# Performance work log

Measured on AMD Instinct MI355X. Metric: run time of the kernel, lower is better.

## Reference

```python
import jax, jax.numpy as jnp
import numpy as np

B, S, K_IN = 8, 2048, 512
D_MODEL, N_INPUT, N_PROCESS = 1024, 4096, 2048
K = 256


def setup_inputs() -> dict:
    key = jax.random.key(0)
    k1, k2, k3, k4 = jax.random.split(key, 4)
    return {
        "selected_activations": jax.random.normal(k1, (B, S, K_IN), dtype=jnp.float32),
        "selected_indices": jax.random.randint(k2, (B, K_IN), 0, N_INPUT, dtype=jnp.int64),
        "k": K,
        "combination_weights": jax.random.normal(k3, (N_PROCESS, N_INPUT), dtype=jnp.float32),
        "output_projections": jax.random.normal(k4, (N_PROCESS, D_MODEL), dtype=jnp.float32),
    }


def reference(selected_activations, selected_indices, k, combination_weights, output_projections):
    # Gather per-batch combination weights: [n_process, B, k_in] -> [B, n_process, k_in]
    sel_w = jnp.take(combination_weights, selected_indices, axis=1)  # [P, B, k_in]
    sel_w = jnp.transpose(sel_w, (1, 0, 2))                          # [B, P, k_in]
    # Batched matmul + exact GELU (torch F.gelu default is erf-based)
    process_act = jax.nn.gelu(
        jnp.einsum("bsk,bpk->bsp", selected_activations, sel_w), approximate=False
    )  # [B, S, P]
    # Top-k gating over mean activation across sequence
    process_scores = process_act.mean(axis=1)                        # [B, P]
    _, proc_idx = jax.lax.top_k(process_scores, k)                   # [B, k]
    # Gather selected process activations along last dim
    sel_proc_act = jnp.take_along_axis(process_act, proc_idx[:, None, :], axis=2)  # [B, S, k]
    # Gather output projections per batch: [B, k, d_model]
    sel_proj = output_projections[proc_idx]                          # [B, k, D]
    return jnp.einsum("bsk,bkd->bsd", sel_proc_act, sel_proj)        # [B, S, D]
```

## Files before the change

kernel.cpp:

```cpp
#include <hip/hip_runtime.h>
#include <hip/hip_bf16.h>
#include <math.h>

#define B_    8
#define S_    2048
#define KIN_  512
#define NIN_  4096
#define P_    2048
#define D_    1024
#define KSEL_ 256

typedef __attribute__((ext_vector_type(8))) short short8;
typedef __attribute__((ext_vector_type(4))) float f32x4;

__device__ __forceinline__ unsigned short f2bf(float f) {
    unsigned u = __float_as_uint(f);
    unsigned r = (u + 0x7fffu + ((u >> 16) & 1u)) >> 16;
    return (unsigned short)r;
}
__device__ __forceinline__ float bf2f(unsigned short h) {
    return __uint_as_float(((unsigned)h) << 16);
}
__device__ __forceinline__ float gelu_exact(float x) {
    return 0.5f * x * (1.0f + erff(x * 0.70710678118654752f));
}
__device__ __forceinline__ void gl2lds16(const void* g, void* l) {
    __builtin_amdgcn_global_load_lds(
        (const __attribute__((address_space(1))) unsigned int*)g,
        (__attribute__((address_space(3))) unsigned int*)l, 16, 0, 0);
}

__global__ __launch_bounds__(256) void prep_kernel(
        const float* __restrict__ A, const float* __restrict__ W,
        const int* __restrict__ idx,
        unsigned short* __restrict__ Ahi, unsigned short* __restrict__ Alo,
        unsigned short* __restrict__ Ghi, unsigned short* __restrict__ Glo) {
    int id = blockIdx.x;
    int t  = threadIdx.x;
    if (id < 1024) {
        int b = id >> 7, rb = id & 127;
        int l = t & 63, wv = t >> 6;
        int lr = l & 15, quad = l >> 4;
        const float* src = A + ((size_t)(b * S_ + rb * 16 + lr)) * KIN_ + quad * 8;
        unsigned short* dh = Ahi + ((size_t)(b * S_ + rb * 16 + lr)) * KIN_ + quad * 8;
        unsigned short* dl = Alo + (size_t)(b * 16) * 65536 + (size_t)rb * 512 + (size_t)l * 8;
        for (int kb = wv; kb < 16; kb += 4) {
            float4 v0 = *(const float4*)(src + kb * 32);
            float4 v1 = *(const float4*)(src + kb * 32 + 4);
            float vv[8] = {v0.x, v0.y, v0.z, v0.w, v1.x, v1.y, v1.z, v1.w};
            short8 h8, l8;
#pragma unroll
            for (int jj = 0; jj < 8; jj++) {
                unsigned short h = f2bf(vv[jj]);
                h8[jj] = (short)h;
                l8[jj] = (short)f2bf(vv[jj] - bf2f(h));
            }
            *(short8*)(dh + kb * 32) = h8;
            *(short8*)(dl + (size_t)kb * 65536) = l8;
        }
    } else {
        int bp = id - 1024;
        int b  = bp >> 11;
        const int* ib = idx + (size_t)b * KIN_;
        const float* wrow = W + (size_t)(bp & 2047) * NIN_;
        size_t o = (size_t)bp * KIN_;
        for (int j = t; j < KIN_; j += 256) {
            float v = wrow[ib[j]];
            unsigned short h = f2bf(v);
            Ghi[o + j] = h;
            Glo[o + j] = f2bf(v - bf2f(h));
        }
    }
}

template <bool STORE_C>
__global__ __launch_bounds__(256, 3) void gemm1_score(
        const unsigned short* __restrict__ Ahi, const unsigned short* __restrict__ Alo,
        const unsigned short* __restrict__ Ghi, const unsigned short* __restrict__ Glo,
        float* __restrict__ scores, unsigned short* __restrict__ C) {
    __shared__ __align__(16) unsigned short lds[24576];

    int d    = blockIdx.x;
    int xcd  = d & 7;
    int slot = d >> 3;
    int c    = (slot >> 4) * 8 + xcd;
    int j    = slot & 15;
    int b    = c >> 4;
    int rc   = c & 15;
    int p0   = ((rc & 3) * 4 + (j & 3)) * 128;
    int s0   = ((rc >> 2) * 4 + (j >> 2)) * 128;

    const int t  = threadIdx.x;
    const int w = t >> 6, l = t & 63;
    const int wm = w & 1, wn = w >> 1;
    const int lr = l & 15, quad = l >> 4;

    const int srow = t >> 2;
    const int koff = ((t & 3) ^ ((t >> 3) & 3)) * 8;
    const size_t baseA = ((size_t)(b * S_ + s0)) * KIN_;
    const size_t baseG = ((size_t)(b * P_ + p0)) * KIN_;
    const unsigned short* pA0 = Ahi + baseA + (size_t)srow * KIN_ + koff;
    const unsigned short* pA1 = pA0 + (size_t)64 * KIN_;
    const unsigned short* pG0 = Ghi + baseG + (size_t)srow * KIN_ + koff;
    const unsigned short* pG1 = pG0 + (size_t)64 * KIN_;
    const unsigned short* pH0 = Glo + baseG + (size_t)srow * KIN_ + koff;
    const unsigned short* pH1 = pH0 + (size_t)64 * KIN_;
    const unsigned short* alB = Alo + (size_t)(b * 16) * 65536
                              + (size_t)((s0 >> 4) + wm * 4) * 512 + (size_t)l * 8;
    char* lb = (char*)lds + w * 1024;

    int ra[4], rg[4];
#pragma unroll
    for (int i = 0; i < 4; i++) {
        int rowa = wm * 64 + i * 16 + lr;
        int rowg = wn * 64 + i * 16 + lr;
        ra[i] = rowa * 32 + (quad ^ ((rowa >> 1) & 3)) * 8;
        rg[i] = rowg * 32 + (quad ^ ((rowg >> 1) & 3)) * 8;
    }

    f32x4 acc[4][4];
#pragma unroll
    for (int i = 0; i < 4; i++)
#pragma unroll
        for (int jj = 0; jj < 4; jj++) acc[i][jj] = (f32x4){0.f, 0.f, 0.f, 0.f};

    auto issue = [&](int k0, int buf) {
        char* dst = lb + buf * 24576;
        gl2lds16(pA0 + k0, dst + 0);
        gl2lds16(pA1 + k0, dst + 4096);
        gl2lds16(pG0 + k0, dst + 8192);
        gl2lds16(pG1 + k0, dst + 12288);
        gl2lds16(pH0 + k0, dst + 16384);
        gl2lds16(pH1 + k0, dst + 20480);
    };

    issue(0, 0);
    for (int it = 0; it < KIN_ / 32; ++it) {
        short8 alc[4];
#pragma unroll
        for (int mt = 0; mt < 4; mt++)
            alc[mt] = *(const short8*)(alB + (size_t)it * 65536 + mt * 512);
        if (it + 1 < KIN_ / 32) {
            issue((it + 1) * 32, (it + 1) & 1);
            asm volatile("s_waitcnt vmcnt(10)\n\ts_barrier" ::: "memory");
        } else {
            asm volatile("s_waitcnt vmcnt(0)\n\ts_barrier" ::: "memory");
        }
        const unsigned short* Lb = lds + (it & 1) * 12288;

        short8 gh[4], gl8[4];
#pragma unroll
        for (int i = 0; i < 4; i++) {
            gh[i]  = *(const short8*)(Lb + 4096 + rg[i]);
            gl8[i] = *(const short8*)(Lb + 8192 + rg[i]);
        }
#pragma unroll
        for (int mt = 0; mt < 4; mt++) {
            short8 ah = *(const short8*)(Lb + ra[mt]);
#pragma unroll
            for (int nt = 0; nt < 4; nt++) {
                acc[mt][nt] = __builtin_amdgcn_mfma_f32_16x16x32_bf16(ah,      gh[nt],  acc[mt][nt], 0, 0, 0);
                acc[mt][nt] = __builtin_amdgcn_mfma_f32_16x16x32_bf16(ah,      gl8[nt], acc[mt][nt], 0, 0, 0);
                acc[mt][nt] = __builtin_amdgcn_mfma_f32_16x16x32_bf16(alc[mt], gh[nt],  acc[mt][nt], 0, 0, 0);
            }
        }
        asm volatile("s_barrier" ::: "memory");
    }

    float colsum[4] = {0.f, 0.f, 0.f, 0.f};
#pragma unroll
    for (int mt = 0; mt < 4; mt++)
#pragma unroll
        for (int nt = 0; nt < 4; nt++)
#pragma unroll
            for (int r = 0; r < 4; r++) {
                float g = gelu_exact(acc[mt][nt][r]);
                colsum[nt] += g;
                acc[mt][nt][r] = g;
            }
#pragma unroll
    for (int nt = 0; nt < 4; nt++) {
        colsum[nt] += __shfl_xor(colsum[nt], 16);
        colsum[nt] += __shfl_xor(colsum[nt], 32);
    }
    if (quad == 0) {
#pragma unroll
        for (int nt = 0; nt < 4; nt++)
            atomicAdd(&scores[b * P_ + p0 + wn * 64 + nt * 16 + lr], colsum[nt]);
    }

    if (STORE_C) {
#pragma unroll
        for (int mt = 0; mt < 4; mt++)
#pragma unroll
            for (int nt = 0; nt < 4; nt++)
#pragma unroll
                for (int r = 0; r < 4; r++) {
                    int row = wm * 64 + mt * 16 + quad * 4 + r;
                    int col = wn * 64 + nt * 16 + lr;
                    lds[row * 128 + col] = f2bf(acc[mt][nt][r]);
                }
        __syncthreads();
        for (int i = t; i < 2048; i += 256) {
            int row = i >> 4, ch = i & 15;
            uint4 v = *(const uint4*)(lds + row * 128 + ch * 8);
            *(uint4*)(C + ((size_t)(b * S_ + s0 + row)) * P_ + p0 + ch * 8) = v;
        }
    }
}

__global__ __launch_bounds__(1024) void topk_kernel(const float* __restrict__ scores,
                                                    int* __restrict__ pidx) {
    __shared__ float v[2048];
    __shared__ int   ix[2048];
    int b = blockIdx.x;
    int t = threadIdx.x;
    for (int i = t; i < 2048; i += 1024) { v[i] = scores[b * 2048 + i]; ix[i] = i; }
    __syncthreads();
    for (int k = 2; k <= 2048; k <<= 1) {
        for (int j = k >> 1; j > 0; j >>= 1) {
            for (int i = t; i < 2048; i += 1024) {
                int o = i ^ j;
                if (o > i) {
                    bool desc = ((i & k) == 0);
                    float va = v[i], vb = v[o];
                    int ia = ix[i], ib = ix[o];
                    bool b_first = (vb > va) || (vb == va && ib < ia);
                    if (desc == b_first) { v[i] = vb; v[o] = va; ix[i] = ib; ix[o] = ia; }
                }
            }
            __syncthreads();
        }
    }
    if (t < KSEL_) pidx[b * KSEL_ + t] = ix[t];
}

__global__ __launch_bounds__(256) void gathers_kernel(
        const unsigned short* __restrict__ C, const float* __restrict__ proj,
        const int* __restrict__ pidx,
        unsigned short* __restrict__ selact, unsigned short* __restrict__ PselT,
        int base) {
    __shared__ int pj[256];
    __shared__ unsigned short tile[64][65];
    int id = blockIdx.x + base, t = threadIdx.x;
    if (id < 2048) {
        int b = id >> 8;
        pj[t] = pidx[b * KSEL_ + t];
        __syncthreads();
        size_t r0 = (size_t)b * S_ + (id & 255) * 8;
#pragma unroll
        for (int r = 0; r < 8; ++r) {
            size_t row = r0 + r;
            selact[row * KSEL_ + t] = C[row * P_ + pj[t]];
        }
    } else {
        int g = id - 2048;
        int d0 = (g & 15) * 64, k0 = ((g >> 4) & 3) * 64, b = g >> 6;
        int tr = t >> 6;
        int tc = t & 63;
#pragma unroll
        for (int r = 0; r < 16; r++) {
            int kk = r * 4 + tr;
            int prow = pidx[b * KSEL_ + k0 + kk];
            tile[kk][tc] = f2bf(proj[(size_t)prow * D_ + d0 + tc]);
        }
        __syncthreads();
#pragma unroll
        for (int r = 0; r < 16; r++) {
            int dd = r * 4 + tr;
            PselT[((size_t)(b * D_ + d0 + dd)) * KSEL_ + k0 + tc] = tile[tc][dd];
        }
    }
}

__global__ __launch_bounds__(256) void gemm1b_selact(
        const unsigned short* __restrict__ Ahi, const unsigned short* __restrict__ Alo,
        const unsigned short* __restrict__ Ghi, const unsigned short* __restrict__ Glo,
        const int* __restrict__ pidx, unsigned short* __restrict__ selact) {
    __shared__ __align__(16) unsigned short lds[16384];

    const int t  = threadIdx.x;
    const int b  = blockIdx.z;
    const int s0 = blockIdx.y * 128;
    const int n0 = blockIdx.x * 128;
    const int w = t >> 6, l = t & 63;
    const int wm = w & 1, wn = w >> 1;
    const int lr = l & 15, quad = l >> 4;

    const int srow = t >> 2;
    const int koff = ((t & 3) ^ ((t >> 3) & 3)) * 8;
    const size_t baseA = ((size_t)(b * S_ + s0)) * KIN_;
    const size_t offA0 = baseA + (size_t)srow * KIN_ + koff;
    const size_t offA1 = offA0 + (size_t)64 * KIN_;
    const int prow0 = pidx[b * KSEL_ + n0 + srow];
    const int prow1 = pidx[b * KSEL_ + n0 + 64 + srow];
    const size_t offG0 = ((size_t)(b * P_ + prow0)) * KIN_ + koff;
    const size_t offG1 = ((size_t)(b * P_ + prow1)) * KIN_ + koff;
    const unsigned short* alB = Alo + (size_t)(b * 16) * 65536
                              + (size_t)((s0 >> 4) + wm * 4) * 512 + (size_t)l * 8;
    char* lb = (char*)lds + w * 1024;

    int ra[4], rg[4];
#pragma unroll
    for (int i = 0; i < 4; i++) {
        int rowa = wm * 64 + i * 16 + lr;
        int rowg = wn * 64 + i * 16 + lr;
        ra[i] = rowa * 32 + (quad ^ ((rowa >> 1) & 3)) * 8;
        rg[i] = rowg * 32 + (quad ^ ((rowg >> 1) & 3)) * 8;
    }

    f32x4 acc[4][4];
#pragma unroll
    for (int i = 0; i < 4; i++)
#pragma unroll
        for (int jj = 0; jj < 4; jj++) acc[i][jj] = (f32x4){0.f, 0.f, 0.f, 0.f};

    for (int k0 = 0; k0 < KIN_; k0 += 32) {
        gl2lds16(Ahi + offA0 + k0, lb + 0);
        gl2lds16(Ahi + offA1 + k0, lb + 4096);
        gl2lds16(Ghi + offG0 + k0, lb + 8192);
        gl2lds16(Ghi + offG1 + k0, lb + 12288);
        gl2lds16(Glo + offG0 + k0, lb + 16384);
        gl2lds16(Glo + offG1 + k0, lb + 20480);
        short8 alc[4];
#pragma unroll
        for (int mt = 0; mt < 4; mt++)
            alc[mt] = *(const short8*)(alB + (size_t)(k0 >> 5) * 65536 + mt * 512);
        __syncthreads();

        short8 gh[4], gl8[4];
#pragma unroll
        for (int i = 0; i < 4; i++) {
            gh[i]  = *(const short8*)(lds + 4096 + rg[i]);
            gl8[i] = *(const short8*)(lds + 8192 + rg[i]);
        }
#pragma unroll
        for (int mt = 0; mt < 4; mt++) {
            short8 ah = *(const short8*)(lds + ra[mt]);
#pragma unroll
            for (int nt = 0; nt < 4; nt++) {
                acc[mt][nt] = __builtin_amdgcn_mfma_f32_16x16x32_bf16(ah,      gh[nt],  acc[mt][nt], 0, 0, 0);
                acc[mt][nt] = __builtin_amdgcn_mfma_f32_16x16x32_bf16(ah,      gl8[nt], acc[mt][nt], 0, 0, 0);
                acc[mt][nt] = __builtin_amdgcn_mfma_f32_16x16x32_bf16(alc[mt], gh[nt],  acc[mt][nt], 0, 0, 0);
            }
        }
        __syncthreads();
    }

#pragma unroll
    for (int mt = 0; mt < 4; mt++)
#pragma unroll
        for (int nt = 0; nt < 4; nt++)
#pragma unroll
            for (int r = 0; r < 4; r++) {
                int row = wm * 64 + mt * 16 + quad * 4 + r;
                int col = wn * 64 + nt * 16 + lr;
                lds[row * 128 + col] = f2bf(gelu_exact(acc[mt][nt][r]));
            }
    __syncthreads();
    for (int i = t; i < 2048; i += 256) {
        int row = i >> 4, ch = i & 15;
        uint4 v = *(const uint4*)(lds + row * 128 + ch * 8);
        *(uint4*)(selact + ((size_t)(b * S_ + s0 + row)) * KSEL_ + n0 + ch * 8) = v;
    }
}

__global__ __launch_bounds__(256) void gemm2_mfma(
        const unsigned short* __restrict__ selact,
        const unsigned short* __restrict__ PselT,
        float* __restrict__ out) {
    __shared__ __align__(16) unsigned short lds[16384];

    const int t  = threadIdx.x;
    const int b  = blockIdx.z;
    const int s0 = blockIdx.y * 128;
    const int d0 = blockIdx.x * 128;
    const int w = t >> 6, l = t & 63;
    const int wm = w & 1, wn = w >> 1;
    const int lr = l & 15, quad = l >> 4;

    const int srow = t >> 2;
    const int koff = ((t & 3) ^ ((t >> 3) & 3)) * 8;
    const unsigned short* pA0 = selact + ((size_t)(b * S_ + s0 + srow)) * KSEL_ + koff;
    const unsigned short* pA1 = pA0 + (size_t)64 * KSEL_;
    const unsigned short* pB0 = PselT + ((size_t)(b * D_ + d0 + srow)) * KSEL_ + koff;
    const unsigned short* pB1 = pB0 + (size_t)64 * KSEL_;
    char* lb = (char*)lds + w * 1024;

    int ra[4], rg[4];
#pragma unroll
    for (int i = 0; i < 4; i++) {
        int rowa = wm * 64 + i * 16 + lr;
        int rowg = wn * 64 + i * 16 + lr;
        ra[i] = rowa * 32 + (quad ^ ((rowa >> 1) & 3)) * 8;
        rg[i] = rowg * 32 + (quad ^ ((rowg >> 1) & 3)) * 8;
    }

    f32x4 acc[4][4];
#pragma unroll
    for (int i = 0; i < 4; i++)
#pragma unroll
        for (int jj = 0; jj < 4; jj++) acc[i][jj] = (f32x4){0.f, 0.f, 0.f, 0.f};

    auto issue = [&](int k0, int buf) {
        char* dst = lb + buf * 16384;
        gl2lds16(pA0 + k0, dst + 0);
        gl2lds16(pA1 + k0, dst + 4096);
        gl2lds16(pB0 + k0, dst + 8192);
        gl2lds16(pB1 + k0, dst + 12288);
    };

    issue(0, 0);
    for (int it = 0; it < KSEL_ / 32; ++it) {
        if (it + 1 < KSEL_ / 32) {
            issue((it + 1) * 32, (it + 1) & 1);
            asm volatile("s_waitcnt vmcnt(4)\n\ts_barrier" ::: "memory");
        } else {
            asm volatile("s_waitcnt vmcnt(0)\n\ts_barrier" ::: "memory");
        }
        const unsigned short* Lb = lds + (it & 1) * 8192;

        short8 af[4], bf[4];
#pragma unroll
        for (int i = 0; i < 4; i++) {
            af[i] = *(const short8*)(Lb + ra[i]);
            bf[i] = *(const short8*)(Lb + 4096 + rg[i]);
        }
#pragma unroll
        for (int mt = 0; mt < 4; mt++)
#pragma unroll
            for (int nt = 0; nt < 4; nt++)
                acc[mt][nt] = __builtin_amdgcn_mfma_f32_16x16x32_bf16(af[mt], bf[nt], acc[mt][nt], 0, 0, 0);
        asm volatile("s_barrier" ::: "memory");
    }

#pragma unroll
    for (int mt = 0; mt < 4; mt++)
#pragma unroll
        for (int nt = 0; nt < 4; nt++)
#pragma unroll
            for (int r = 0; r < 4; r++)
                out[((size_t)(b * S_ + s0 + wm * 64 + mt * 16 + quad * 4 + r)) * D_
                    + d0 + wn * 64 + nt * 16 + lr] = acc[mt][nt][r];
}

extern "C" void kernel_launch(void* const* d_in, const int* in_sizes, int n_in,
                              void* d_out, int out_size, void* d_ws, size_t ws_size,
                              hipStream_t stream) {
    (void)in_sizes; (void)n_in; (void)out_size;
    const float* act  = (const float*)d_in[0];
    const int*   idx  = (const int*)d_in[1];
    const float* W    = (const float*)d_in[3];
    const float* proj = (const float*)d_in[4];
    float*       out  = (float*)d_out;

    char* ws = (char*)d_ws;
    unsigned short* Ahi    = (unsigned short*)(ws + 0);
    unsigned short* Alo    = (unsigned short*)(ws + 16777216);
    unsigned short* Ghi    = (unsigned short*)(ws + 33554432);
    unsigned short* Glo    = (unsigned short*)(ws + 50331648);
    float*          scores = (float*)(ws + 67108864);
    int*            pidx   = (int*)(ws + 67174400);
    unsigned short* selact = (unsigned short*)(ws + 67182592);
    unsigned short* PselT  = (unsigned short*)(ws + 75571200);
    unsigned short* Cbf    = (unsigned short*)(ws + 79765504);
    const bool big = ws_size >= 146874368ull;

    hipMemsetAsync(scores, 0, B_ * P_ * sizeof(float), stream);

    prep_kernel<<<dim3(1024 + B_ * P_), 256, 0, stream>>>(act, W, idx, Ahi, Alo, Ghi, Glo);

    if (big) {
        gemm1_score<true><<<dim3(2048), 256, 0, stream>>>(Ahi, Alo, Ghi, Glo, scores, Cbf);
        topk_kernel<<<dim3(B_), 1024, 0, stream>>>(scores, pidx);
        gathers_kernel<<<dim3(2048 + 512), 256, 0, stream>>>(Cbf, proj, pidx, selact, PselT, 0);
    } else {
        gemm1_score<false><<<dim3(2048), 256, 0, stream>>>(Ahi, Alo, Ghi, Glo, scores, nullptr);
        topk_kernel<<<dim3(B_), 1024, 0, stream>>>(scores, pidx);
        gemm1b_selact<<<dim3(KSEL_ / 128, S_ / 128, B_), 256, 0, stream>>>(
            Ahi, Alo, Ghi, Glo, pidx, selact);
        gathers_kernel<<<dim3(512), 256, 0, stream>>>(Cbf, proj, pidx, selact, PselT, 2048);
    }
    gemm2_mfma<<<dim3(D_ / 128, S_ / 128, B_), 256, 0, stream>>>(selact, PselT, out);
}
```

Measured before the change: 364.0 us.

## Store G low-part in MFMA fragment layout and load it directly to registers

```diff
diff --git a/kernel.cpp b/kernel.cpp
--- a/kernel.cpp
+++ b/kernel.cpp
@@ -30,11 +30,13 @@
         (__attribute__((address_space(3))) unsigned int*)l, 16, 0, 0);
 }
 
+
 __global__ __launch_bounds__(256) void prep_kernel(
         const float* __restrict__ A, const float* __restrict__ W,
         const int* __restrict__ idx,
-        unsigned short* __restrict__ Ahi, unsigned short* __restrict__ Alo,
-        unsigned short* __restrict__ Ghi, unsigned short* __restrict__ Glo) {
+        unsigned short* __restrict__ Ahi, unsigned short* __restrict__ AloF,
+        unsigned short* __restrict__ Ghi, unsigned short* __restrict__ GloF) {
+    __shared__ int ibs[KIN_];
     int id = blockIdx.x;
     int t  = threadIdx.x;
     if (id < 1024) {
@@ -43,7 +45,7 @@
         int lr = l & 15, quad = l >> 4;
         const float* src = A + ((size_t)(b * S_ + rb * 16 + lr)) * KIN_ + quad * 8;
         unsigned short* dh = Ahi + ((size_t)(b * S_ + rb * 16 + lr)) * KIN_ + quad * 8;
-        unsigned short* dl = Alo + (size_t)(b * 16) * 65536 + (size_t)rb * 512 + (size_t)l * 8;
+        unsigned short* dl = AloF + (size_t)b * 1048576 + (size_t)rb * 512 + (size_t)l * 8;
         for (int kb = wv; kb < 16; kb += 4) {
             float4 v0 = *(const float4*)(src + kb * 32);
             float4 v1 = *(const float4*)(src + kb * 32 + 4);
@@ -59,26 +61,37 @@
             *(short8*)(dl + (size_t)kb * 65536) = l8;
         }
     } else {
-        int bp = id - 1024;
-        int b  = bp >> 11;
-        const int* ib = idx + (size_t)b * KIN_;
-        const float* wrow = W + (size_t)(bp & 2047) * NIN_;
-        size_t o = (size_t)bp * KIN_;
-        for (int j = t; j < KIN_; j += 256) {
-            float v = wrow[ib[j]];
+        int g = id - 1024;
+        int b = g >> 9;
+        ibs[t]       = idx[b * KIN_ + t];
+        ibs[t + 256] = idx[b * KIN_ + t + 256];
+        __syncthreads();
+        int wv = t >> 6, tt = t & 63;
+        int p  = (g * 4 + wv) & 2047;
+        const float* wrow = W + (size_t)p * NIN_;
+        size_t o = ((size_t)b * P_ + p) * KIN_;
+        unsigned short* gf = GloF + (size_t)b * 1048576 + (size_t)(tt >> 2) * 65536
+                           + (size_t)(p >> 4) * 512
+                           + (size_t)((tt & 3) * 16 + (p & 15)) * 8;
+        short8 h8, l8;
+#pragma unroll
+        for (int e = 0; e < 8; e++) {
+            float v = wrow[ibs[tt * 8 + e]];
             unsigned short h = f2bf(v);
-            Ghi[o + j] = h;
-            Glo[o + j] = f2bf(v - bf2f(h));
-        }
+            h8[e] = (short)h;
+            l8[e] = (short)f2bf(v - bf2f(h));
+        }
+        *(short8*)(Ghi + o + tt * 8) = h8;
+        *(short8*)gf = l8;
     }
 }
 
 template <bool STORE_C>
-__global__ __launch_bounds__(256, 3) void gemm1_score(
-        const unsigned short* __restrict__ Ahi, const unsigned short* __restrict__ Alo,
-        const unsigned short* __restrict__ Ghi, const unsigned short* __restrict__ Glo,
+__global__ __launch_bounds__(256, 4) void gemm1_score(
+        const unsigned short* __restrict__ Ahi, const unsigned short* __restrict__ AloF,
+        const unsigned short* __restrict__ Ghi, const unsigned short* __restrict__ GloF,
         float* __restrict__ scores, unsigned short* __restrict__ C) {
-    __shared__ __align__(16) unsigned short lds[24576];
+    __shared__ __align__(16) unsigned short lds[16384];
 
     int d    = blockIdx.x;
     int xcd  = d & 7;
@@ -103,10 +116,10 @@
     const unsigned short* pA1 = pA0 + (size_t)64 * KIN_;
     const unsigned short* pG0 = Ghi + baseG + (size_t)srow * KIN_ + koff;
     const unsigned short* pG1 = pG0 + (size_t)64 * KIN_;
-    const unsigned short* pH0 = Glo + baseG + (size_t)srow * KIN_ + koff;
-    const unsigned short* pH1 = pH0 + (size_t)64 * KIN_;
-    const unsigned short* alB = Alo + (size_t)(b * 16) * 65536
+    const unsigned short* alB = AloF + (size_t)b * 1048576
                               + (size_t)((s0 >> 4) + wm * 4) * 512 + (size_t)l * 8;
+    const unsigned short* glB = GloF + (size_t)b * 1048576
+                              + (size_t)((p0 >> 4) + wn * 4) * 512 + (size_t)l * 8;
     char* lb = (char*)lds + w * 1024;
 
     int ra[4], rg[4];
@@ -125,42 +138,39 @@
         for (int jj = 0; jj < 4; jj++) acc[i][jj] = (f32x4){0.f, 0.f, 0.f, 0.f};
 
     auto issue = [&](int k0, int buf) {
-        char* dst = lb + buf * 24576;
+        char* dst = lb + buf * 16384;
         gl2lds16(pA0 + k0, dst + 0);
         gl2lds16(pA1 + k0, dst + 4096);
         gl2lds16(pG0 + k0, dst + 8192);
         gl2lds16(pG1 + k0, dst + 12288);
-        gl2lds16(pH0 + k0, dst + 16384);
-        gl2lds16(pH1 + k0, dst + 20480);
     };
 
     issue(0, 0);
     for (int it = 0; it < KIN_ / 32; ++it) {
-        short8 alc[4];
-#pragma unroll
-        for (int mt = 0; mt < 4; mt++)
-            alc[mt] = *(const short8*)(alB + (size_t)it * 65536 + mt * 512);
+        short8 alc[4], glc[4];
+#pragma unroll
+        for (int i = 0; i < 4; i++) {
+            alc[i] = *(const short8*)(alB + (size_t)it * 65536 + i * 512);
+            glc[i] = *(const short8*)(glB + (size_t)it * 65536 + i * 512);
+        }
         if (it + 1 < KIN_ / 32) {
             issue((it + 1) * 32, (it + 1) & 1);
-            asm volatile("s_waitcnt vmcnt(10)\n\ts_barrier" ::: "memory");
+            asm volatile("s_waitcnt vmcnt(12)\n\ts_barrier" ::: "memory");
         } else {
-            asm volatile("s_waitcnt vmcnt(0)\n\ts_barrier" ::: "memory");
-        }
-        const unsigned short* Lb = lds + (it & 1) * 12288;
-
-        short8 gh[4], gl8[4];
-#pragma unroll
-        for (int i = 0; i < 4; i++) {
-            gh[i]  = *(const short8*)(Lb + 4096 + rg[i]);
-            gl8[i] = *(const short8*)(Lb + 8192 + rg[i]);
-        }
+            asm volatile("s_waitcnt vmcnt(8)\n\ts_barrier" ::: "memory");
+        }
+        const unsigned short* Lb = lds + (it & 1) * 8192;
+
+        short8 gh[4];
+#pragma unroll
+        for (int i = 0; i < 4; i++) gh[i] = *(const short8*)(Lb + 4096 + rg[i]);
 #pragma unroll
         for (int mt = 0; mt < 4; mt++) {
             short8 ah = *(const short8*)(Lb + ra[mt]);
 #pragma unroll
             for (int nt = 0; nt < 4; nt++) {
                 acc[mt][nt] = __builtin_amdgcn_mfma_f32_16x16x32_bf16(ah,      gh[nt],  acc[mt][nt], 0, 0, 0);
-                acc[mt][nt] = __builtin_amdgcn_mfma_f32_16x16x32_bf16(ah,      gl8[nt], acc[mt][nt], 0, 0, 0);
+                acc[mt][nt] = __builtin_amdgcn_mfma_f32_16x16x32_bf16(ah,      glc[nt], acc[mt][nt], 0, 0, 0);
                 acc[mt][nt] = __builtin_amdgcn_mfma_f32_16x16x32_bf16(alc[mt], gh[nt],  acc[mt][nt], 0, 0, 0);
             }
         }
@@ -274,8 +284,8 @@
 }
 
 __global__ __launch_bounds__(256) void gemm1b_selact(
-        const unsigned short* __restrict__ Ahi, const unsigned short* __restrict__ Alo,
-        const unsigned short* __restrict__ Ghi, const unsigned short* __restrict__ Glo,
+        const unsigned short* __restrict__ Ahi, const unsigned short* __restrict__ AloF,
+        const unsigned short* __restrict__ Ghi, const unsigned short* __restrict__ GloF,
         const int* __restrict__ pidx, unsigned short* __restrict__ selact) {
     __shared__ __align__(16) unsigned short lds[16384];
 
@@ -296,8 +306,15 @@
     const int prow1 = pidx[b * KSEL_ + n0 + 64 + srow];
     const size_t offG0 = ((size_t)(b * P_ + prow0)) * KIN_ + koff;
     const size_t offG1 = ((size_t)(b * P_ + prow1)) * KIN_ + koff;
-    const unsigned short* alB = Alo + (size_t)(b * 16) * 65536
+    const unsigned short* alB = AloF + (size_t)b * 1048576
                               + (size_t)((s0 >> 4) + wm * 4) * 512 + (size_t)l * 8;
+    const unsigned short* glb = GloF + (size_t)b * 1048576;
+    size_t gloff[4];
+#pragma unroll
+    for (int i = 0; i < 4; i++) {
+        int pp = pidx[b * KSEL_ + n0 + wn * 64 + i * 16 + lr];
+        gloff[i] = (size_t)(pp >> 4) * 512 + (size_t)(quad * 16 + (pp & 15)) * 8;
+    }
     char* lb = (char*)lds + w * 1024;
 
     int ra[4], rg[4];
@@ -316,31 +333,29 @@
         for (int jj = 0; jj < 4; jj++) acc[i][jj] = (f32x4){0.f, 0.f, 0.f, 0.f};
 
     for (int k0 = 0; k0 < KIN_; k0 += 32) {
+        int kb = k0 >> 5;
         gl2lds16(Ahi + offA0 + k0, lb + 0);
         gl2lds16(Ahi + offA1 + k0, lb + 4096);
         gl2lds16(Ghi + offG0 + k0, lb + 8192);
         gl2lds16(Ghi + offG1 + k0, lb + 12288);
-        gl2lds16(Glo + offG0 + k0, lb + 16384);
-        gl2lds16(Glo + offG1 + k0, lb + 20480);
-        short8 alc[4];
-#pragma unroll
-        for (int mt = 0; mt < 4; mt++)
-            alc[mt] = *(const short8*)(alB + (size_t)(k0 >> 5) * 65536 + mt * 512);
+        short8 alc[4], glc[4];
+#pragma unroll
+        for (int i = 0; i < 4; i++) {
+            alc[i] = *(const short8*)(alB + (size_t)kb * 65536 + i * 512);
+            glc[i] = *(const short8*)(glb + (size_t)kb * 65536 + gloff[i]);
+        }
         __syncthreads();
 
-        short8 gh[4], gl8[4];
-#pragma unroll
-        for (int i = 0; i < 4; i++) {
-            gh[i]  = *(const short8*)(lds + 4096 + rg[i]);
-            gl8[i] = *(const short8*)(lds + 8192 + rg[i]);
-        }
+        short8 gh[4];
+#pragma unroll
+        for (int i = 0; i < 4; i++) gh[i] = *(const short8*)(lds + 4096 + rg[i]);
 #pragma unroll
         for (int mt = 0; mt < 4; mt++) {
             short8 ah = *(const short8*)(lds + ra[mt]);
 #pragma unroll
             for (int nt = 0; nt < 4; nt++) {
                 acc[mt][nt] = __builtin_amdgcn_mfma_f32_16x16x32_bf16(ah,      gh[nt],  acc[mt][nt], 0, 0, 0);
-                acc[mt][nt] = __builtin_amdgcn_mfma_f32_16x16x32_bf16(ah,      gl8[nt], acc[mt][nt], 0, 0, 0);
+                acc[mt][nt] = __builtin_amdgcn_mfma_f32_16x16x32_bf16(ah,      glc[nt], acc[mt][nt], 0, 0, 0);
                 acc[mt][nt] = __builtin_amdgcn_mfma_f32_16x16x32_bf16(alc[mt], gh[nt],  acc[mt][nt], 0, 0, 0);
             }
         }
@@ -365,7 +380,7 @@
     }
 }
 
-__global__ __launch_bounds__(256) void gemm2_mfma(
+__global__ __launch_bounds__(256, 4) void gemm2_mfma(
         const unsigned short* __restrict__ selact,
         const unsigned short* __restrict__ PselT,
         float* __restrict__ out) {
@@ -456,9 +471,9 @@
 
     char* ws = (char*)d_ws;
     unsigned short* Ahi    = (unsigned short*)(ws + 0);
-    unsigned short* Alo    = (unsigned short*)(ws + 16777216);
+    unsigned short* AloF   = (unsigned short*)(ws + 16777216);
     unsigned short* Ghi    = (unsigned short*)(ws + 33554432);
-    unsigned short* Glo    = (unsigned short*)(ws + 50331648);
+    unsigned short* GloF   = (unsigned short*)(ws + 50331648);
     float*          scores = (float*)(ws + 67108864);
     int*            pidx   = (int*)(ws + 67174400);
     unsigned short* selact = (unsigned short*)(ws + 67182592);
@@ -468,17 +483,17 @@
 
     hipMemsetAsync(scores, 0, B_ * P_ * sizeof(float), stream);
 
-    prep_kernel<<<dim3(1024 + B_ * P_), 256, 0, stream>>>(act, W, idx, Ahi, Alo, Ghi, Glo);
+    prep_kernel<<<dim3(1024 + (B_ * P_) / 4), 256, 0, stream>>>(act, W, idx, Ahi, AloF, Ghi, GloF);
 
     if (big) {
-        gemm1_score<true><<<dim3(2048), 256, 0, stream>>>(Ahi, Alo, Ghi, Glo, scores, Cbf);
+        gemm1_score<true><<<dim3(2048), 256, 0, stream>>>(Ahi, AloF, Ghi, GloF, scores, Cbf);
         topk_kernel<<<dim3(B_), 1024, 0, stream>>>(scores, pidx);
         gathers_kernel<<<dim3(2048 + 512), 256, 0, stream>>>(Cbf, proj, pidx, selact, PselT, 0);
     } else {
-        gemm1_score<false><<<dim3(2048), 256, 0, stream>>>(Ahi, Alo, Ghi, Glo, scores, nullptr);
+        gemm1_score<false><<<dim3(2048), 256, 0, stream>>>(Ahi, AloF, Ghi, GloF, scores, nullptr);
         topk_kernel<<<dim3(B_), 1024, 0, stream>>>(scores, pidx);
         gemm1b_selact<<<dim3(KSEL_ / 128, S_ / 128, B_), 256, 0, stream>>>(
-            Ahi, Alo, Ghi, Glo, pidx, selact);
+            Ahi, AloF, Ghi, GloF, pidx, selact);
         gathers_kernel<<<dim3(512), 256, 0, stream>>>(Cbf, proj, pidx, selact, PselT, 2048);
     }
     gemm2_mfma<<<dim3(D_ / 128, S_ / 128, B_), 256, 0, stream>>>(selact, PselT, out);
```

Result: slower. 396.8 us (+9.0%).
